# Optimization experiments

Measured on AMD Instinct MI355X. Metric: run time of the kernel, lower is better.

The kernel has to match this reference:

```python
import jax, jax.numpy as jnp
import numpy as np

B, S, N_LM, MAX_LEN = 32, 384, 543, 384

_FACE = [33, 133, 362, 263, 61, 291, 199, 419, 17, 84, 314, 405, 320, 307, 375, 321, 308, 324, 318]
_SEL = np.array(_FACE + list(range(468, 489)) + list(range(522, 543)) + [11, 12, 13, 14, 15, 16], dtype=np.int32)  # 67 landmarks
# pairwise distance index pairs: i in range(3), j in i+1..min(i+3, L)
_PAIRS = [(0, 1), (0, 2), (1, 2), (1, 3), (2, 3), (2, 4)]


def setup_inputs() -> dict:
    key = jax.random.key(0)
    x = jax.random.normal(key, (B, S, N_LM, 3), dtype=jnp.float32)
    return {"x": x}


def _safe_norm(v):
    # torch.norm(v + 1e-8, dim=-1, keepdim=True)
    w = v + 1e-8
    return jnp.sqrt(jnp.sum(w * w, axis=-1, keepdims=True))


def reference(x):
    # select 67 landmarks, keep xy only (z never enters the feature stack)
    c = x[:, :, _SEL, :2]                                  # (B,S,67,2)
    # per-frame masked mean-centering (inputs are finite -> plain mean)
    c = c - jnp.mean(c, axis=2, keepdims=True)
    # per-frame std over flattened (L*2) values, unbiased (torch.std)
    bsz, seq, L, _ = c.shape
    std = jnp.std(c.reshape(bsz, seq, -1), axis=-1, ddof=1)  # (B,S)
    scale = jnp.where(std > 1e-6, 1.0 / std, 1.0)[:, :, None, None]
    c = c * scale                                          # (B,S,67,2)

    zrow = jnp.zeros((bsz, 1, L, 2), c.dtype)
    vel = jnp.concatenate([zrow, c[:, 1:] - c[:, :-1]], axis=1)
    acc = jnp.concatenate([jnp.zeros((bsz, 2, L, 2), c.dtype), vel[:, 2:] - vel[:, 1:-1]], axis=1)

    vm = _safe_norm(vel)                                   # (B,S,67,1)
    am = _safe_norm(acc)
    # cum[t] = sum_{k<t} vm[k]
    cum = jnp.concatenate([jnp.zeros((bsz, 1, L, 1), c.dtype), jnp.cumsum(vm[:, :-1], axis=1)], axis=1)

    ang = jnp.arctan2(vel[..., 1:2] + 1e-8, vel[..., 0:1] + 1e-8)
    dchg = jnp.concatenate([jnp.zeros((bsz, 2, L, 1), c.dtype), ang[:, 2:] - ang[:, 1:-1]], axis=1)

    dists = jnp.concatenate([_safe_norm(c[:, :, i] - c[:, :, j]) for i, j in _PAIRS], axis=-1)  # (B,S,6)

    flat = lambda a: a.reshape(bsz, seq, -1)
    feats = jnp.concatenate([flat(c), flat(vel), flat(acc), flat(vm), flat(am), flat(cum), flat(ang), flat(dchg), dists], axis=-1)
    feats = jnp.where(jnp.isfinite(feats), feats, 0.0)
    return feats[:, :MAX_LEN]
```

## Files before the change

kernel.cpp:

```cpp
#include <hip/hip_runtime.h>
#include <math.h>

#define NB 32
#define NS 384
#define NLM 543
#define NL 67
#define NF 743

__constant__ int d_SEL[NL] = {
    33, 133, 362, 263, 61, 291, 199, 419, 17, 84, 314, 405, 320, 307, 375, 321, 308, 324, 318,
    468, 469, 470, 471, 472, 473, 474, 475, 476, 477, 478, 479, 480, 481, 482, 483, 484, 485, 486, 487, 488,
    522, 523, 524, 525, 526, 527, 528, 529, 530, 531, 532, 533, 534, 535, 536, 537, 538, 539, 540, 541, 542,
    11, 12, 13, 14, 15, 16
};

__device__ __forceinline__ float fin(float v) { return isfinite(v) ? v : 0.0f; }


__device__ __forceinline__ void gather_norm(const float* __restrict__ xr,
                                            int lane, int o0, int o1, bool has1,
                                            float& c0x, float& c0y,
                                            float& c1x, float& c1y) {
    float a0x = xr[o0], a0y = xr[o0 + 1];
    float a1x = 0.f, a1y = 0.f;
    if (has1) { a1x = xr[o1]; a1y = xr[o1 + 1]; }

    float sx = a0x + a1x, sy = a0y + a1y;
    #pragma unroll
    for (int off = 32; off; off >>= 1) { sx += __shfl_xor(sx, off); sy += __shfl_xor(sy, off); }
    const float mx = sx * (1.0f / 67.0f), my = sy * (1.0f / 67.0f);

    c0x = a0x - mx; c0y = a0y - my;
    c1x = a1x - mx; c1y = a1y - my;

    float ss = c0x * c0x + c0y * c0y + (has1 ? (c1x * c1x + c1y * c1y) : 0.f);
    #pragma unroll
    for (int off = 32; off; off >>= 1) ss += __shfl_xor(ss, off);
    const float stdv = sqrtf(ss * (1.0f / 133.0f));
    const float scale = (stdv > 1e-6f) ? (1.0f / stdv) : 1.0f;

    c0x *= scale; c0y *= scale; c1x *= scale; c1y *= scale;
}

__global__ __launch_bounds__(256) void k_main(const float* __restrict__ x,
                                              float* __restrict__ out,
                                              float* __restrict__ vmstage) {
    const int wave = threadIdx.x >> 6;
    const int lane = threadIdx.x & 63;
    const int bs = blockIdx.x * 4 + wave;
    const int s = bs % NS;
    const int b = bs / NS;

    const int lm0 = lane;
    const bool has1 = (lane < 3);
    const int lm1 = lane + 64;
    const int o0 = d_SEL[lm0] * 3;
    const int o1 = has1 ? d_SEL[lm1] * 3 : 0;

    const float* __restrict__ xr = x + (size_t)bs * (NLM * 3);

    float c0x, c0y, c1x, c1y;
    gather_norm(xr, lane, o0, o1, has1, c0x, c0y, c1x, c1y);

    float p0x = 0.f, p0y = 0.f, p1x = 0.f, p1y = 0.f;
    if (s >= 1) gather_norm(xr - NLM * 3, lane, o0, o1, has1, p0x, p0y, p1x, p1y);
    float q0x = 0.f, q0y = 0.f, q1x = 0.f, q1y = 0.f;
    if (s >= 2) gather_norm(xr - 2 * NLM * 3, lane, o0, o1, has1, q0x, q0y, q1x, q1y);

    float* __restrict__ row = out + (size_t)bs * NF;

    #pragma unroll
    for (int half = 0; half < 2; ++half) {
        if (half == 1 && !has1) break;
        const int lm  = half ? lm1 : lm0;
        const float cx = half ? c1x : c0x, cy = half ? c1y : c0y;
        const float px = half ? p1x : p0x, py = half ? p1y : p0y;
        const float qx = half ? q1x : q0x, qy = half ? q1y : q0y;

        const float vx = (s >= 1) ? (cx - px) : 0.f;
        const float vy = (s >= 1) ? (cy - py) : 0.f;
        const float v1x = px - qx, v1y = py - qy;
        const float ax = (s >= 2) ? (vx - v1x) : 0.f;
        const float ay = (s >= 2) ? (vy - v1y) : 0.f;

        const float wx = vx + 1e-8f, wy = vy + 1e-8f;
        const float vm = sqrtf(wx * wx + wy * wy);
        const float ux = ax + 1e-8f, uy = ay + 1e-8f;
        const float am = sqrtf(ux * ux + uy * uy);

        const float ang = atan2f(vy + 1e-8f, vx + 1e-8f);
        float dchg = 0.f;
        if (s >= 2) dchg = ang - atan2f(v1y + 1e-8f, v1x + 1e-8f);

        row[2 * lm]       = fin(cx);
        row[2 * lm + 1]   = fin(cy);
        row[134 + 2 * lm] = vx;
        row[135 + 2 * lm] = vy;
        row[268 + 2 * lm] = ax;
        row[269 + 2 * lm] = ay;
        row[402 + lm]     = vm;
        row[469 + lm]     = am;
        row[603 + lm]     = fin(ang);
        row[670 + lm]     = fin(dchg);
        vmstage[((size_t)b * NL + lm) * NS + s] = vm;
    }

    const int PI_[6] = {0, 0, 1, 1, 2, 2};
    const int PJ_[6] = {1, 2, 2, 3, 3, 4};
    const int p = (lane < 6) ? lane : 0;
    float xi = __shfl(c0x, PI_[p]); float yi = __shfl(c0y, PI_[p]);
    float xj = __shfl(c0x, PJ_[p]); float yj = __shfl(c0y, PJ_[p]);
    if (lane < 6) {
        float dx = xi - xj + 1e-8f, dy = yi - yj + 1e-8f;
        row[737 + lane] = fin(sqrtf(dx * dx + dy * dy));
    }
}

__global__ __launch_bounds__(256) void k_scan(const float* __restrict__ vmstage,
                                              float* __restrict__ out) {
    const int gw = (int)((blockIdx.x * 256u + threadIdx.x) >> 6);
    const int lane = threadIdx.x & 63;
    const int b = gw / NL;
    const int lm = gw - b * NL;
    const float* __restrict__ src = vmstage + (size_t)gw * NS;

    float carry = 0.f;
    #pragma unroll
    for (int k = 0; k < 6; ++k) {
        const int t = k * 64 + lane;
        const float v = src[t];
        float incl = v;
        #pragma unroll
        for (int off = 1; off < 64; off <<= 1) {
            float y = __shfl_up(incl, off);
            if (lane >= off) incl += y;
        }
        out[((size_t)(b * NS + t)) * NF + 536 + lm] = fin(carry + (incl - v));
        carry += __shfl(incl, 63);
    }
}

extern "C" void kernel_launch(void* const* d_in, const int* in_sizes, int n_in,
                              void* d_out, int out_size, void* d_ws, size_t ws_size,
                              hipStream_t stream) {
    const float* x = (const float*)d_in[0];
    float* out = (float*)d_out;
    float* vmstage = (float*)d_ws;

    k_main<<<(NB * NS) / 4, 256, 0, stream>>>(x, out, vmstage);
    k_scan<<<(NB * NL) / 4, 256, 0, stream>>>(vmstage, out);
}
```

Measured before the change: 136.5 us.

## Share normalized frames across waves via LDS and scan velocity magnitudes from output

Each block now covers four consecutive frames of one batch. Each wave normalizes only its own frame and writes it to shared memory, and two waves also compute the two preceding halo frames. This replaces the three gather-and-normalize passes each wave did before. The vm staging buffer is removed: the cumulative-sum kernel reads vm back from the output rows and runs a sequential 384-step scan per landmark thread. That scan uses only 32 blocks with a long serial dependency chain, so it risks being latency-bound.

```diff
diff --git a/kernel.cpp b/kernel.cpp
--- a/kernel.cpp
+++ b/kernel.cpp
@@ -18,7 +18,7 @@
 
 
 __device__ __forceinline__ void gather_norm(const float* __restrict__ xr,
-                                            int lane, int o0, int o1, bool has1,
+                                            int o0, int o1, bool has1,
                                             float& c0x, float& c0y,
                                             float& c1x, float& c1y) {
     float a0x = xr[o0], a0y = xr[o0 + 1];
@@ -43,13 +43,15 @@
 }
 
 __global__ __launch_bounds__(256) void k_main(const float* __restrict__ x,
-                                              float* __restrict__ out,
-                                              float* __restrict__ vmstage) {
+                                              float* __restrict__ out) {
+    __shared__ float2 csh[6][NL];
+
     const int wave = threadIdx.x >> 6;
     const int lane = threadIdx.x & 63;
-    const int bs = blockIdx.x * 4 + wave;
-    const int s = bs % NS;
-    const int b = bs / NS;
+    const int b = blockIdx.x / 96;
+    const int s_base = (blockIdx.x - b * 96) * 4;
+    const int s = s_base + wave;
+    const int bs = b * NS + s;
 
     const int lm0 = lane;
     const bool has1 = (lane < 3);
@@ -57,29 +59,50 @@
     const int o0 = d_SEL[lm0] * 3;
     const int o1 = has1 ? d_SEL[lm1] * 3 : 0;
 
-    const float* __restrict__ xr = x + (size_t)bs * (NLM * 3);
+    const float* __restrict__ xb = x + (size_t)(b * NS) * (NLM * 3);
 
     float c0x, c0y, c1x, c1y;
-    gather_norm(xr, lane, o0, o1, has1, c0x, c0y, c1x, c1y);
+    gather_norm(xb + (size_t)s * (NLM * 3), o0, o1, has1, c0x, c0y, c1x, c1y);
+    csh[wave + 2][lm0] = make_float2(c0x, c0y);
+    if (has1) csh[wave + 2][lm1] = make_float2(c1x, c1y);
 
-    float p0x = 0.f, p0y = 0.f, p1x = 0.f, p1y = 0.f;
-    if (s >= 1) gather_norm(xr - NLM * 3, lane, o0, o1, has1, p0x, p0y, p1x, p1y);
-    float q0x = 0.f, q0y = 0.f, q1x = 0.f, q1y = 0.f;
-    if (s >= 2) gather_norm(xr - 2 * NLM * 3, lane, o0, o1, has1, q0x, q0y, q1x, q1y);
+    if (wave == 0) {
+        if (s_base >= 1) {
+            float bx, by, b1x, b1y;
+            gather_norm(xb + (size_t)(s_base - 1) * (NLM * 3), o0, o1, has1, bx, by, b1x, b1y);
+            csh[1][lm0] = make_float2(bx, by);
+            if (has1) csh[1][lm1] = make_float2(b1x, b1y);
+        } else {
+            csh[1][lm0] = make_float2(0.f, 0.f);
+            if (has1) csh[1][lm1] = make_float2(0.f, 0.f);
+        }
+    }
+    if (wave == 1) {
+        if (s_base >= 2) {
+            float bx, by, b1x, b1y;
+            gather_norm(xb + (size_t)(s_base - 2) * (NLM * 3), o0, o1, has1, bx, by, b1x, b1y);
+            csh[0][lm0] = make_float2(bx, by);
+            if (has1) csh[0][lm1] = make_float2(b1x, b1y);
+        } else {
+            csh[0][lm0] = make_float2(0.f, 0.f);
+            if (has1) csh[0][lm1] = make_float2(0.f, 0.f);
+        }
+    }
+    __syncthreads();
 
     float* __restrict__ row = out + (size_t)bs * NF;
 
     #pragma unroll
     for (int half = 0; half < 2; ++half) {
         if (half == 1 && !has1) break;
-        const int lm  = half ? lm1 : lm0;
+        const int lm = half ? lm1 : lm0;
         const float cx = half ? c1x : c0x, cy = half ? c1y : c0y;
-        const float px = half ? p1x : p0x, py = half ? p1y : p0y;
-        const float qx = half ? q1x : q0x, qy = half ? q1y : q0y;
+        const float2 p = csh[wave + 1][lm];
+        const float2 q = csh[wave][lm];
 
-        const float vx = (s >= 1) ? (cx - px) : 0.f;
-        const float vy = (s >= 1) ? (cy - py) : 0.f;
-        const float v1x = px - qx, v1y = py - qy;
+        const float vx = (s >= 1) ? (cx - p.x) : 0.f;
+        const float vy = (s >= 1) ? (cy - p.y) : 0.f;
+        const float v1x = p.x - q.x, v1y = p.y - q.y;
         const float ax = (s >= 2) ? (vx - v1x) : 0.f;
         const float ay = (s >= 2) ? (vy - v1y) : 0.f;
 
@@ -102,7 +125,6 @@
         row[469 + lm]     = am;
         row[603 + lm]     = fin(ang);
         row[670 + lm]     = fin(dchg);
-        vmstage[((size_t)b * NL + lm) * NS + s] = vm;
     }
 
     const int PI_[6] = {0, 0, 1, 1, 2, 2};
@@ -116,27 +138,17 @@
     }
 }
 
-__global__ __launch_bounds__(256) void k_scan(const float* __restrict__ vmstage,
-                                              float* __restrict__ out) {
-    const int gw = (int)((blockIdx.x * 256u + threadIdx.x) >> 6);
-    const int lane = threadIdx.x & 63;
-    const int b = gw / NL;
-    const int lm = gw - b * NL;
-    const float* __restrict__ src = vmstage + (size_t)gw * NS;
+__global__ __launch_bounds__(128) void k_scan(float* __restrict__ out) {
+    const int b = blockIdx.x;
+    const int t = threadIdx.x;
+    if (t >= NL) return;
 
-    float carry = 0.f;
-    #pragma unroll
-    for (int k = 0; k < 6; ++k) {
-        const int t = k * 64 + lane;
-        const float v = src[t];
-        float incl = v;
-        #pragma unroll
-        for (int off = 1; off < 64; off <<= 1) {
-            float y = __shfl_up(incl, off);
-            if (lane >= off) incl += y;
-        }
-        out[((size_t)(b * NS + t)) * NF + 536 + lm] = fin(carry + (incl - v));
-        carry += __shfl(incl, 63);
+    float acc = 0.f;
+    #pragma unroll 8
+    for (int s = 0; s < NS; ++s) {
+        float* row = out + (size_t)(b * NS + s) * NF;
+        row[536 + t] = fin(acc);
+        acc += row[402 + t];
     }
 }
 
@@ -145,8 +157,7 @@
                               hipStream_t stream) {
     const float* x = (const float*)d_in[0];
     float* out = (float*)d_out;
-    float* vmstage = (float*)d_ws;
 
-    k_main<<<(NB * NS) / 4, 256, 0, stream>>>(x, out, vmstage);
-    k_scan<<<(NB * NL) / 4, 256, 0, stream>>>(vmstage, out);
+    k_main<<<NB * (NS / 4), 256, 0, stream>>>(x, out);
+    k_scan<<<NB, 128, 0, stream>>>(out);
 }
```

Result: slower. 153.9 us (+12.8%).
